# Kernel tuning notes

Measured on AMD Instinct MI355X. Metric: run time of the kernel, lower is better.

Reference implementation:

```python
import jax, jax.numpy as jnp
import numpy as np

VOCAB, D, S, T, B, E, C = 21128, 768, 50, 5, 512, 128, 10


def gcn(x, edges, W, b):
    # GCNConv with self-loops and symmetric normalization. x: [S, D]
    N = x.shape[0]
    loop = jnp.arange(N)
    src = jnp.concatenate([edges[0], loop])
    dst = jnp.concatenate([edges[1], loop])
    deg = jax.ops.segment_sum(jnp.ones_like(src, dtype=x.dtype), dst, num_segments=N)
    dinv = jax.lax.rsqrt(jnp.maximum(deg, 1e-12))
    norm = dinv[src] * dinv[dst]
    h = x @ W  # [S, 10]
    out = jax.ops.segment_sum(h[src] * norm[:, None], dst, num_segments=N)
    return out + b


def mpm(self_f, cross_f, assign, W1, b1, W2, b2):
    # multi-perspective matching, broadcast over leading dims; node dim = -2
    a = assign * self_f
    c = assign * cross_f
    num = jnp.sum(a * c, axis=-1)
    den = jnp.maximum(jnp.linalg.norm(a, axis=-1) * jnp.linalg.norm(c, axis=-1), 1e-8)
    cos = num / den
    bshape = jnp.broadcast_shapes(self_f.shape[:-2], cross_f.shape[:-2])
    sf = jnp.broadcast_to(self_f, bshape + self_f.shape[-2:])
    h = jnp.concatenate([cos[..., None], sf], axis=-1)  # [..., S, 11]
    h = jax.nn.relu(h @ W1 + b1) @ W2 + b2  # [..., S, 20]
    return jnp.max(h, axis=-2)  # [..., 20]


def setup_inputs() -> dict:
    key = jax.random.key(0)
    ks = jax.random.split(key, 20)
    inp = {
        "context_input": jax.random.randint(ks[0], (B, T, S), 0, VOCAB),
        "response_input": jax.random.randint(ks[1], (B, S), 0, VOCAB),
        "context_graph_adjs": jax.random.randint(ks[2], (B, T, 2, E), 0, S),
        "response_graph_adj": jax.random.randint(ks[3], (B, 2, E), 0, S),
        "word_emb": jax.random.normal(ks[4], (VOCAB, D), jnp.float32) * 0.02,
        "conv_W": jax.random.normal(ks[5], (D, C), jnp.float32) * 0.05,
        "conv_b": jnp.zeros((C,), jnp.float32),
        "cross_w": jax.random.uniform(ks[6], (D, C), jnp.float32),
        "attention_coef": jax.random.uniform(ks[7], (S, S), jnp.float32),
        "assign_weight": jax.random.uniform(ks[8], (S, C), jnp.float32),
        "mp_W1": jax.random.normal(ks[9], (C + 1, 20), jnp.float32) * 0.3,
        "mp_b1": jnp.zeros((20,), jnp.float32),
        "mp_W2": jax.random.normal(ks[10], (20, 20), jnp.float32) * 0.2,
        "mp_b2": jnp.zeros((20,), jnp.float32),
        "ffn_W1": jax.random.normal(ks[11], (80, 40), jnp.float32) * 0.1,
        "ffn_b1": jnp.zeros((40,), jnp.float32),
        "ffn_W2": jax.random.normal(ks[12], (40, 1), jnp.float32) * 0.2,
        "ffn_b2": jnp.zeros((1,), jnp.float32),
    }
    return inp


def reference(context_input, response_input, context_graph_adjs, response_graph_adj,
              word_emb, conv_W, conv_b, cross_w, attention_coef, assign_weight,
              mp_W1, mp_b1, mp_W2, mp_b2, ffn_W1, ffn_b1, ffn_W2, ffn_b2):
    ctx = word_emb[context_input]      # [B, T, S, D]
    resp = word_emb[response_input]    # [B, S, D]

    gcn_b = jax.vmap(gcn, in_axes=(0, 0, None, None))
    resp_gcn = gcn_b(resp, response_graph_adj, conv_W, conv_b)                      # [B, S, C]
    ctx_gcn = jax.vmap(gcn_b, in_axes=(0, 0, None, None))(ctx, context_graph_adjs, conv_W, conv_b)  # [B, T, S, C]

    # cross features: utterance cross comes from response, response cross from utterance
    u_cross = jnp.einsum('ps,bsk->bpk', attention_coef, resp @ cross_w)   # [B, S, C]
    r_cross = jnp.einsum('ps,btsk->btpk', attention_coef, ctx @ cross_w)  # [B, T, S, C]

    g_u = mpm(ctx_gcn, u_cross[:, None], assign_weight, mp_W1, mp_b1, mp_W2, mp_b2)       # [B, T, 20]
    g_r = mpm(resp_gcn[:, None], r_cross, assign_weight, mp_W1, mp_b1, mp_W2, mp_b2)      # [B, T, 20]

    feat = jnp.concatenate([g_u, g_r, g_u * g_r, jnp.abs(g_u - g_r)], axis=-1)  # [B, T, 80]
    logits = jax.nn.relu(feat @ ffn_W1 + ffn_b1) @ ffn_W2 + ffn_b2              # [B, T, 1]
    return jax.nn.sigmoid(jnp.sum(logits, axis=1))                              # [B, 1]
```

## Files before the change

### kernel.cpp

```cpp
#include <hip/hip_runtime.h>
#include <math.h>

#define VOCAB 21128
#define DD 768
#define SS 50
#define TT 5
#define BB 512
#define EE 128
#define CC 10
#define V20 (VOCAB * 20)
#define NG 2560
#define NALL 3072

__global__ __launch_bounds__(512) void k_vocab(const float* __restrict__ emb,
                                               const float* __restrict__ Wconv,
                                               const float* __restrict__ Wcross,
                                               float* __restrict__ hvp) {
    __shared__ float tile[8][64][21];
    const int wv = threadIdx.x >> 6, lane = threadIdx.x & 63;
    const int rowbase = blockIdx.x * 64;
    const int rsub = lane >> 2, m = lane & 3;

    const int d0w = blockIdx.y * 384 + __builtin_amdgcn_readfirstlane(wv * 48);

    float4 v[12];
#pragma unroll
    for (int ch = 0; ch < 3; ++ch) {
#pragma unroll
        for (int it = 0; it < 4; ++it) {
            int row = it * 16 + rsub;
            long r = rowbase + row;
            if (r >= VOCAB) r = VOCAB - 1;
            v[ch * 4 + it] = *(const float4*)(emb + r * DD + d0w + ch * 16 + m * 4);
        }
    }

    float acc[20];
#pragma unroll
    for (int c = 0; c < 20; c++) acc[c] = 0.f;

#pragma unroll
    for (int ch = 0; ch < 3; ++ch) {
        const int d0 = d0w + ch * 16;
#pragma unroll
        for (int it = 0; it < 4; ++it) {
            const int row = it * 16 + rsub;
            const float4 w = v[ch * 4 + it];
            tile[wv][row][m * 4 + 0] = w.x;
            tile[wv][row][m * 4 + 1] = w.y;
            tile[wv][row][m * 4 + 2] = w.z;
            tile[wv][row][m * 4 + 3] = w.w;
        }
#pragma unroll
        for (int d = 0; d < 16; ++d) {
            float e = tile[wv][lane][d];
            const float* wc = Wconv + (d0 + d) * 10;
            const float* wx = Wcross + (d0 + d) * 10;
#pragma unroll
            for (int c = 0; c < 10; c++) {
                acc[c] = fmaf(e, wc[c], acc[c]);
                acc[10 + c] = fmaf(e, wx[c], acc[10 + c]);
            }
        }
    }

    __syncthreads();
    float* pp = &tile[0][0][0];
#pragma unroll
    for (int c = 0; c < 20; c++) pp[wv * 1280 + lane * 20 + c] = acc[c];
    __syncthreads();
    float* outp = hvp + (long)blockIdx.y * V20;
    for (int i = threadIdx.x; i < 1280; i += 512) {
        int row = i / 20;
        long r = rowbase + row;
        if (r < VOCAB) {
            float s = 0.f;
#pragma unroll
            for (int w = 0; w < 8; ++w) s += pp[w * 1280 + i];
            outp[r * 20 + (i - row * 20)] = s;
        }
    }
}

__global__ __launch_bounds__(256) void k_gcn(const int* __restrict__ ctok,
                                             const int* __restrict__ cadj,
                                             const int* __restrict__ rtok,
                                             const int* __restrict__ radj,
                                             const float* __restrict__ hvp,
                                             const float* __restrict__ convb,
                                             const float* __restrict__ att,
                                             float* __restrict__ P) {
    __shared__ float attT[SS][51];
    __shared__ float hcv[4][SS][12];
    __shared__ float hcx[4][SS][12];
    __shared__ float aggL[4][SS][11];
    __shared__ int dgS[4][64];
    const int tid = threadIdx.x, wv = tid >> 6, lane = tid & 63;
    const int G = blockIdx.x * 4 + wv;

    for (int i = tid; i < SS * SS; i += 256) { int p = i / SS, s = i - p * SS; attT[s][p] = att[i]; }
    __syncthreads();

    const int* tb;
    const int* ab;
    if (G < NG) { tb = ctok + (long)G * SS; ab = cadj + (long)G * 2 * EE; }
    else        { int b = G - NG; tb = rtok + (long)b * SS; ab = radj + (long)b * 2 * EE; }

    const int e1s = ab[lane], e2s = ab[lane + 64];
    const int e1d = ab[EE + lane], e2d = ab[EE + lane + 64];
    const int myTok = (lane < SS) ? tb[lane] : 0;

    dgS[wv][lane] = 0;
    atomicAdd(&dgS[wv][e1d], 1);
    atomicAdd(&dgS[wv][e2d], 1);

    const float4* hv4 = (const float4*)hvp;
#pragma unroll
    for (int it = 0; it < 4; ++it) {
        const int idx = it * 64 + lane;
        int row = idx / 5;
        const int q = idx - row * 5;
        const int rowc = (row < SS) ? row : (SS - 1);
        const int t = __shfl(myTok, rowc);
        if (idx < SS * 5) {
            const float4 a = hv4[(long)t * 5 + q];
            const float4 b = hv4[(long)(VOCAB * 5) + (long)t * 5 + q];
            const float4 w = make_float4(a.x + b.x, a.y + b.y, a.z + b.z, a.w + b.w);
            if (q == 0)      *(float4*)&hcv[wv][row][0] = w;
            else if (q == 1) *(float4*)&hcv[wv][row][4] = w;
            else if (q == 2) { hcv[wv][row][8] = w.x; hcv[wv][row][9] = w.y;
                               hcx[wv][row][0] = w.z; hcx[wv][row][1] = w.w; }
            else if (q == 3) { *(float2*)&hcx[wv][row][2] = make_float2(w.x, w.y);
                               *(float2*)&hcx[wv][row][4] = make_float2(w.z, w.w); }
            else             { *(float2*)&hcx[wv][row][6] = make_float2(w.x, w.y);
                               *(float2*)&hcx[wv][row][8] = make_float2(w.z, w.w); }
        }
    }

    float dv = 0.f;
    if (lane < SS) dv = rsqrtf((float)(dgS[wv][lane] + 1));

    float* aggW = &aggL[wv][0][0];
    for (int i = lane; i < SS * 11; i += 64) aggW[i] = 0.f;
    const float n1 = __shfl(dv, e1s) * __shfl(dv, e1d);
    const float n2 = __shfl(dv, e2s) * __shfl(dv, e2d);
#pragma unroll
    for (int c = 0; c < CC; c++) atomicAdd(&aggW[e1d * 11 + c], hcv[wv][e1s][c] * n1);
#pragma unroll
    for (int c = 0; c < CC; c++) atomicAdd(&aggW[e2d * 11 + c], hcv[wv][e2s][c] * n2);

    const int pc = (lane < SS) ? lane : (SS - 1);
    float xo[CC];
#pragma unroll
    for (int c = 0; c < CC; c++) xo[c] = hcx[wv][pc][c];

    const int p = lane;
    if (p < SS) {
        float gcn[CC];
        const float dp2 = dv * dv;
        const float4 s0 = *(const float4*)&hcv[wv][p][0];
        const float4 s1 = *(const float4*)&hcv[wv][p][4];
        const float s8 = hcv[wv][p][8], s9 = hcv[wv][p][9];
        gcn[0] = aggW[p * 11 + 0] + s0.x * dp2 + convb[0];
        gcn[1] = aggW[p * 11 + 1] + s0.y * dp2 + convb[1];
        gcn[2] = aggW[p * 11 + 2] + s0.z * dp2 + convb[2];
        gcn[3] = aggW[p * 11 + 3] + s0.w * dp2 + convb[3];
        gcn[4] = aggW[p * 11 + 4] + s1.x * dp2 + convb[4];
        gcn[5] = aggW[p * 11 + 5] + s1.y * dp2 + convb[5];
        gcn[6] = aggW[p * 11 + 6] + s1.z * dp2 + convb[6];
        gcn[7] = aggW[p * 11 + 7] + s1.w * dp2 + convb[7];
        gcn[8] = aggW[p * 11 + 8] + s8 * dp2 + convb[8];
        gcn[9] = aggW[p * 11 + 9] + s9 * dp2 + convb[9];

        float ax[CC];
#pragma unroll
        for (int c = 0; c < CC; c++) ax[c] = 0.f;
#pragma unroll 5
        for (int s = 0; s < SS; ++s) {
            const float a = attT[s][p];
#pragma unroll
            for (int c = 0; c < CC; c++) {
                const float xs = __uint_as_float(
                    __builtin_amdgcn_readlane(__float_as_uint(xo[c]), s));
                ax[c] = fmaf(a, xs, ax[c]);
            }
        }
        float4* o4 = (float4*)(P + (long)G * 1000 + p * 20);
        o4[0] = make_float4(gcn[0], gcn[1], gcn[2], gcn[3]);
        o4[1] = make_float4(gcn[4], gcn[5], gcn[6], gcn[7]);
        o4[2] = make_float4(gcn[8], gcn[9], ax[0], ax[1]);
        o4[3] = make_float4(ax[2], ax[3], ax[4], ax[5]);
        o4[4] = make_float4(ax[6], ax[7], ax[8], ax[9]);
    }
}

__global__ __launch_bounds__(256) void k_mpm(const float* __restrict__ P,
                                             const float* __restrict__ assign,
                                             const float* __restrict__ W1, const float* __restrict__ b1,
                                             const float* __restrict__ W2, const float* __restrict__ b2,
                                             float* __restrict__ guG,
                                             float* __restrict__ grG) {
    __shared__ float W2T[20][21];
    __shared__ float asgL[SS][11];
    __shared__ float h1L[4][SS][20];
    const int tid = threadIdx.x, wv = tid >> 6, lane = tid & 63;
    const int wid = blockIdx.x * 4 + wv;
    const int g = wid >> 1, which = wid & 1;
    const int b = g / TT;

    for (int i = tid; i < 400; i += 256) W2T[i % 20][i / 20] = W2[i];
    for (int i = tid; i < SS * CC; i += 256) asgL[i / CC][i % CC] = assign[i];
    __syncthreads();

    const float* Pc = P + (long)g * 1000;
    const float* Pr = P + (long)(NG + b) * 1000;
    const float* selfP = which ? Pr : Pc;
    const float* croP  = which ? Pc : Pr;

    const int p = lane;
    float self[CC], cro[CC];
    if (p < SS) {
        const float4* s4 = (const float4*)(selfP + p * 20);
        const float4 a0 = s4[0], a1 = s4[1], a2 = s4[2];
        self[0] = a0.x; self[1] = a0.y; self[2] = a0.z; self[3] = a0.w;
        self[4] = a1.x; self[5] = a1.y; self[6] = a1.z; self[7] = a1.w;
        self[8] = a2.x; self[9] = a2.y;
        const float4* c4 = (const float4*)(croP + p * 20);
        const float4 b0 = c4[2], b1q = c4[3], b2q = c4[4];
        cro[0] = b0.z; cro[1] = b0.w;
        cro[2] = b1q.x; cro[3] = b1q.y; cro[4] = b1q.z; cro[5] = b1q.w;
        cro[6] = b2q.x; cro[7] = b2q.y; cro[8] = b2q.z; cro[9] = b2q.w;
    }

    const int j = lane % 20;
    const int grp = lane / 20;
    float w2r[20];
#pragma unroll
    for (int k = 0; k < 20; k++) w2r[k] = W2T[j][k];

    if (p < SS) {
        float num = 0.f, na = 0.f, nc2 = 0.f;
#pragma unroll
        for (int c = 0; c < CC; c++) {
            float av = asgL[p][c];
            float a = av * self[c];
            float cx = av * cro[c];
            num = fmaf(a, cx, num);
            na = fmaf(a, a, na);
            nc2 = fmaf(cx, cx, nc2);
        }
        float cosv = num / fmaxf(sqrtf(na) * sqrtf(nc2), 1e-8f);
        float h1[20];
#pragma unroll
        for (int q = 0; q < 20; q++) h1[q] = fmaf(cosv, W1[q], b1[q]);
#pragma unroll
        for (int k = 0; k < CC; k++) {
            float sv = self[k];
#pragma unroll
            for (int q = 0; q < 20; q++) h1[q] = fmaf(sv, W1[(k + 1) * 20 + q], h1[q]);
        }
        float4* hw = (float4*)&h1L[wv][p][0];
        hw[0] = make_float4(fmaxf(h1[0], 0.f), fmaxf(h1[1], 0.f), fmaxf(h1[2], 0.f), fmaxf(h1[3], 0.f));
        hw[1] = make_float4(fmaxf(h1[4], 0.f), fmaxf(h1[5], 0.f), fmaxf(h1[6], 0.f), fmaxf(h1[7], 0.f));
        hw[2] = make_float4(fmaxf(h1[8], 0.f), fmaxf(h1[9], 0.f), fmaxf(h1[10], 0.f), fmaxf(h1[11], 0.f));
        hw[3] = make_float4(fmaxf(h1[12], 0.f), fmaxf(h1[13], 0.f), fmaxf(h1[14], 0.f), fmaxf(h1[15], 0.f));
        hw[4] = make_float4(fmaxf(h1[16], 0.f), fmaxf(h1[17], 0.f), fmaxf(h1[18], 0.f), fmaxf(h1[19], 0.f));
    }

    float part = -1e30f;
    if (grp < 3) {
        const int s0 = grp * 17;
        const int s1 = (grp == 2) ? SS : (s0 + 17);
        for (int s = s0; s < s1; ++s) {
            const float* hr = &h1L[wv][s][0];
            float t = 0.f;
#pragma unroll
            for (int k = 0; k < 20; k++) t = fmaf(hr[k], w2r[k], t);
            part = fmaxf(part, t);
        }
    }
    const float a0 = __shfl(part, j);
    const float a1 = __shfl(part, j + 20);
    const float a2 = __shfl(part, j + 40);
    if (lane < 20) {
        float h2 = fmaxf(fmaxf(a0, a1), a2) + b2[lane];
        (which ? grG : guG)[(long)g * 20 + lane] = h2;
    }
}

__global__ __launch_bounds__(64) void k_final(const float* __restrict__ g_u, const float* __restrict__ g_r,
                                              const float* __restrict__ W1, const float* __restrict__ b1,
                                              const float* __restrict__ W2, const float* __restrict__ b2,
                                              float* __restrict__ out) {
    const int b = blockIdx.x, lane = threadIdx.x;
    float ssum = 0.f;
    for (int t = 0; t < TT; t++) {
        const float* gu = g_u + ((long)b * TT + t) * 20;
        const float* gr = g_r + ((long)b * TT + t) * 20;
        float feat[80];
#pragma unroll
        for (int k = 0; k < 20; k++) {
            float u = gu[k], r = gr[k];
            feat[k] = u;
            feat[20 + k] = r;
            feat[40 + k] = u * r;
            feat[60 + k] = fabsf(u - r);
        }
        if (lane < 40) {
            float hv = b1[lane];
#pragma unroll
            for (int k = 0; k < 80; k++) hv = fmaf(feat[k], W1[k * 40 + lane], hv);
            ssum += fmaxf(hv, 0.f) * W2[lane];
        }
    }
    for (int off = 32; off; off >>= 1) ssum += __shfl_xor(ssum, off);
    if (lane == 0) out[b] = 1.f / (1.f + expf(-(ssum + (float)TT * b2[0])));
}

extern "C" void kernel_launch(void* const* d_in, const int* in_sizes, int n_in,
                              void* d_out, int out_size, void* d_ws, size_t ws_size,
                              hipStream_t stream) {
    (void)in_sizes; (void)n_in; (void)out_size; (void)ws_size;
    const int* ctx_tok = (const int*)d_in[0];
    const int* resp_tok = (const int*)d_in[1];
    const int* ctx_adj = (const int*)d_in[2];
    const int* resp_adj = (const int*)d_in[3];
    const float* emb = (const float*)d_in[4];
    const float* convW = (const float*)d_in[5];
    const float* convb = (const float*)d_in[6];
    const float* crossW = (const float*)d_in[7];
    const float* att = (const float*)d_in[8];
    const float* assign = (const float*)d_in[9];
    const float* mpW1 = (const float*)d_in[10];
    const float* mpb1 = (const float*)d_in[11];
    const float* mpW2 = (const float*)d_in[12];
    const float* mpb2 = (const float*)d_in[13];
    const float* fW1 = (const float*)d_in[14];
    const float* fb1 = (const float*)d_in[15];
    const float* fW2 = (const float*)d_in[16];
    const float* fb2 = (const float*)d_in[17];

    float* ws = (float*)d_ws;
    float* hvp = ws;
    float* P = hvp + 2 * V20;
    float* guG = P + (long)NALL * 1000;
    float* grG = guG + (long)NG * 20;
    float* outf = (float*)d_out;

    hipLaunchKernelGGL(k_vocab, dim3((VOCAB + 63) / 64, 2), dim3(512), 0, stream,
                       emb, convW, crossW, hvp);
    hipLaunchKernelGGL(k_gcn, dim3(NALL / 4), dim3(256), 0, stream,
                       ctx_tok, ctx_adj, resp_tok, resp_adj, hvp, convb, att, P);
    hipLaunchKernelGGL(k_mpm, dim3(NG * 2 / 4), dim3(256), 0, stream,
                       P, assign, mpW1, mpb1, mpW2, mpb2, guG, grG);
    hipLaunchKernelGGL(k_final, dim3(BB), dim3(64), 0, stream,
                       guG, grG, fW1, fb1, fW2, fb2, outf);
}
```

Before: 80.00 us.

## Fuse MPM and final FFN per batch; pre-transpose attention in a prep kernel

```diff
diff --git a/kernel.cpp b/kernel.cpp
--- a/kernel.cpp
+++ b/kernel.cpp
@@ -12,6 +12,14 @@
 #define NG 2560
 #define NALL 3072
 
+__global__ void k_prep(const float* __restrict__ att, float* __restrict__ attG) {
+    int i = blockIdx.x * 64 + threadIdx.x;
+    if (i < SS * SS) {
+        int p = i / SS, s = i - p * SS;
+        attG[s * 52 + p] = att[i];
+    }
+}
+
 __global__ __launch_bounds__(512) void k_vocab(const float* __restrict__ emb,
                                                const float* __restrict__ Wconv,
                                                const float* __restrict__ Wcross,
@@ -88,18 +96,14 @@
                                              const int* __restrict__ radj,
                                              const float* __restrict__ hvp,
                                              const float* __restrict__ convb,
-                                             const float* __restrict__ att,
+                                             const float* __restrict__ attG,
                                              float* __restrict__ P) {
-    __shared__ float attT[SS][51];
     __shared__ float hcv[4][SS][12];
     __shared__ float hcx[4][SS][12];
     __shared__ float aggL[4][SS][11];
     __shared__ int dgS[4][64];
     const int tid = threadIdx.x, wv = tid >> 6, lane = tid & 63;
     const int G = blockIdx.x * 4 + wv;
-
-    for (int i = tid; i < SS * SS; i += 256) { int p = i / SS, s = i - p * SS; attT[s][p] = att[i]; }
-    __syncthreads();
 
     const int* tb;
     const int* ab;
@@ -177,7 +181,7 @@
         for (int c = 0; c < CC; c++) ax[c] = 0.f;
 #pragma unroll 5
         for (int s = 0; s < SS; ++s) {
-            const float a = attT[s][p];
+            const float a = attG[s * 52 + p];
 #pragma unroll
             for (int c = 0; c < CC; c++) {
                 const float xs = __uint_as_float(
@@ -194,22 +198,26 @@
     }
 }
 
-__global__ __launch_bounds__(256) void k_mpm(const float* __restrict__ P,
-                                             const float* __restrict__ assign,
-                                             const float* __restrict__ W1, const float* __restrict__ b1,
-                                             const float* __restrict__ W2, const float* __restrict__ b2,
-                                             float* __restrict__ guG,
-                                             float* __restrict__ grG) {
+__global__ __launch_bounds__(640) void k_mpmf(const float* __restrict__ P,
+                                              const float* __restrict__ assign,
+                                              const float* __restrict__ W1, const float* __restrict__ b1,
+                                              const float* __restrict__ W2, const float* __restrict__ b2,
+                                              const float* __restrict__ fW1, const float* __restrict__ fb1,
+                                              const float* __restrict__ fW2, const float* __restrict__ fb2,
+                                              float* __restrict__ out) {
     __shared__ float W2T[20][21];
     __shared__ float asgL[SS][11];
-    __shared__ float h1L[4][SS][20];
+    __shared__ float h1L[10][SS][20];
+    __shared__ float guS[TT][20];
+    __shared__ float grS[TT][20];
+    __shared__ float fsum[256];
     const int tid = threadIdx.x, wv = tid >> 6, lane = tid & 63;
-    const int wid = blockIdx.x * 4 + wv;
-    const int g = wid >> 1, which = wid & 1;
-    const int b = g / TT;
-
-    for (int i = tid; i < 400; i += 256) W2T[i % 20][i / 20] = W2[i];
-    for (int i = tid; i < SS * CC; i += 256) asgL[i / CC][i % CC] = assign[i];
+    const int b = blockIdx.x;
+    const int t = wv >> 1, which = wv & 1;
+    const int g = b * TT + t;
+
+    for (int i = tid; i < 400; i += 640) W2T[i % 20][i / 20] = W2[i];
+    for (int i = tid; i < SS * CC; i += 640) asgL[i / CC][i % CC] = assign[i];
     __syncthreads();
 
     const float* Pc = P + (long)g * 1000;
@@ -273,10 +281,10 @@
         const int s1 = (grp == 2) ? SS : (s0 + 17);
         for (int s = s0; s < s1; ++s) {
             const float* hr = &h1L[wv][s][0];
-            float t = 0.f;
-#pragma unroll
-            for (int k = 0; k < 20; k++) t = fmaf(hr[k], w2r[k], t);
-            part = fmaxf(part, t);
+            float tt = 0.f;
+#pragma unroll
+            for (int k = 0; k < 20; k++) tt = fmaf(hr[k], w2r[k], tt);
+            part = fmaxf(part, tt);
         }
     }
     const float a0 = __shfl(part, j);
@@ -284,37 +292,32 @@
     const float a2 = __shfl(part, j + 40);
     if (lane < 20) {
         float h2 = fmaxf(fmaxf(a0, a1), a2) + b2[lane];
-        (which ? grG : guG)[(long)g * 20 + lane] = h2;
-    }
-}
-
-__global__ __launch_bounds__(64) void k_final(const float* __restrict__ g_u, const float* __restrict__ g_r,
-                                              const float* __restrict__ W1, const float* __restrict__ b1,
-                                              const float* __restrict__ W2, const float* __restrict__ b2,
-                                              float* __restrict__ out) {
-    const int b = blockIdx.x, lane = threadIdx.x;
-    float ssum = 0.f;
-    for (int t = 0; t < TT; t++) {
-        const float* gu = g_u + ((long)b * TT + t) * 20;
-        const float* gr = g_r + ((long)b * TT + t) * 20;
-        float feat[80];
+        (which ? grS[t] : guS[t])[lane] = h2;
+    }
+    __syncthreads();
+
+    float term = 0.f;
+    if (tid < 200) {
+        const int tt = tid / 40, jj = tid - tt * 40;
+        float hvv = fb1[jj];
 #pragma unroll
         for (int k = 0; k < 20; k++) {
-            float u = gu[k], r = gr[k];
-            feat[k] = u;
-            feat[20 + k] = r;
-            feat[40 + k] = u * r;
-            feat[60 + k] = fabsf(u - r);
-        }
-        if (lane < 40) {
-            float hv = b1[lane];
-#pragma unroll
-            for (int k = 0; k < 80; k++) hv = fmaf(feat[k], W1[k * 40 + lane], hv);
-            ssum += fmaxf(hv, 0.f) * W2[lane];
-        }
-    }
-    for (int off = 32; off; off >>= 1) ssum += __shfl_xor(ssum, off);
-    if (lane == 0) out[b] = 1.f / (1.f + expf(-(ssum + (float)TT * b2[0])));
+            float u = guS[tt][k], r = grS[tt][k];
+            hvv = fmaf(u, fW1[k * 40 + jj], hvv);
+            hvv = fmaf(r, fW1[(20 + k) * 40 + jj], hvv);
+            hvv = fmaf(u * r, fW1[(40 + k) * 40 + jj], hvv);
+            hvv = fmaf(fabsf(u - r), fW1[(60 + k) * 40 + jj], hvv);
+        }
+        term = fmaxf(hvv, 0.f) * fW2[jj];
+    }
+    if (tid < 256) fsum[tid] = term;
+    __syncthreads();
+    if (wv == 0) {
+        float s = fsum[lane] + fsum[lane + 64] + fsum[lane + 128] + fsum[lane + 192];
+#pragma unroll
+        for (int o = 32; o; o >>= 1) s += __shfl_xor(s, o);
+        if (lane == 0) out[b] = 1.f / (1.f + expf(-(s + (float)TT * fb2[0])));
+    }
 }
 
 extern "C" void kernel_launch(void* const* d_in, const int* in_sizes, int n_in,
@@ -343,16 +346,14 @@
     float* ws = (float*)d_ws;
     float* hvp = ws;
     float* P = hvp + 2 * V20;
-    float* guG = P + (long)NALL * 1000;
-    float* grG = guG + (long)NG * 20;
+    float* attG = P + (long)NALL * 1000;
     float* outf = (float*)d_out;
 
+    hipLaunchKernelGGL(k_prep, dim3(40), dim3(64), 0, stream, att, attG);
     hipLaunchKernelGGL(k_vocab, dim3((VOCAB + 63) / 64, 2), dim3(512), 0, stream,
                        emb, convW, crossW, hvp);
     hipLaunchKernelGGL(k_gcn, dim3(NALL / 4), dim3(256), 0, stream,
-                       ctx_tok, ctx_adj, resp_tok, resp_adj, hvp, convb, att, P);
-    hipLaunchKernelGGL(k_mpm, dim3(NG * 2 / 4), dim3(256), 0, stream,
-                       P, assign, mpW1, mpb1, mpW2, mpb2, guG, grG);
-    hipLaunchKernelGGL(k_final, dim3(BB), dim3(64), 0, stream,
-                       guG, grG, fW1, fb1, fW2, fb2, outf);
-}
+                       ctx_tok, ctx_adj, resp_tok, resp_adj, hvp, convb, attG, P);
+    hipLaunchKernelGGL(k_mpmf, dim3(BB), dim3(640), 0, stream,
+                       P, assign, mpW1, mpb1, mpW2, mpb2, fW1, fb1, fW2, fb2, outf);
+}
```

Result: faster. 76.38 us (-4.5%).
